# Kernel tuning notes

Measured on AMD Instinct MI355X. Metric: run time of the kernel, lower is better.

## Reference

```python
import jax, jax.numpy as jnp
import numpy as np

B, T, D = 4, 8192, 1024
N_PROTO = 8


def setup_inputs() -> dict:
    key = jax.random.key(0)
    k1, k2, k3 = jax.random.split(key, 3)
    x = jax.random.normal(k1, (B, T, D), dtype=jnp.float32)
    # torch Linear kaiming-uniform scale ~ 1/sqrt(fan_in); keeps tanh unsaturated
    W = jax.random.normal(k2, (6, D), dtype=jnp.float32) * (1.0 / np.sqrt(D))
    prototypes = jax.random.normal(k3, (N_PROTO, 6), dtype=jnp.float32)
    hamming_scale = jnp.float32(0.1)
    return {"x": x, "W": W, "prototypes": prototypes, "hamming_scale": hamming_scale}


def reference(x, W, prototypes, hamming_scale):
    # q6_project: tanh(Linear(x)) then L2-normalize with clamp(min=1e-6)
    z = jnp.tanh(jnp.einsum('btd,kd->btk', x, W))            # (B,T,6)
    z = z / jnp.clip(jnp.linalg.norm(z, axis=-1, keepdims=True), 1e-6)
    # F.normalize(prototypes, dim=-1) with eps=1e-12
    p = prototypes / jnp.clip(jnp.linalg.norm(prototypes, axis=-1, keepdims=True), 1e-12)
    dot = jnp.einsum('btk,pk->btp', z, p)                    # (B,T,P)
    dist = (6.0 - dot * 6.0) * 0.5                            # Theorem-3 Hamming distance
    return jax.nn.softmax(-hamming_scale * dist, axis=-1)    # routing weights (B,T,P)
```

## Files before the change

### kernel.cpp

```cpp
#include <hip/hip_runtime.h>


#define DIM 1024
#define NK 6
#define NPROTO 8
#define TPI 4

__global__ __launch_bounds__(256, 3) void q6_fused_kernel(
    const float* __restrict__ x,
    const float* __restrict__ W,
    const float* __restrict__ protos,
    const float* __restrict__ hs_ptr,
    float* __restrict__ out,
    int n_tokens, int n_waves)
{
    const int tid  = threadIdx.x;
    const int lane = tid & 63;
    const int wave_id = blockIdx.x * (blockDim.x >> 6) + (tid >> 6);

    __shared__ float4 wlds[NK * (DIM / 4)];
#pragma unroll
    for (int i = 0; i < (NK * DIM / 4) / 256; ++i)
        wlds[i * 256 + tid] = reinterpret_cast<const float4*>(W)[i * 256 + tid];

    const int pl = lane & 7;
    float p[NK];
#pragma unroll
    for (int k = 0; k < NK; ++k) p[k] = protos[pl * NK + k];
    {
        float pn = sqrtf(p[0]*p[0] + p[1]*p[1] + p[2]*p[2] + p[3]*p[3] + p[4]*p[4] + p[5]*p[5]);
        float inv = 1.0f / fmaxf(pn, 1e-12f);
#pragma unroll
        for (int k = 0; k < NK; ++k) p[k] *= inv;
    }
    const float hs = hs_ptr[0];

    __syncthreads();

    const bool hi5 = (lane & 32) != 0;
    const bool hi4 = (lane & 16) != 0;
    const int tloc = lane >> 4;
    const int pidx = lane & 15;

    for (int tb = wave_id * TPI; tb < n_tokens; tb += n_waves * TPI) {
        float4 xv[TPI][4];
#pragma unroll
        for (int t = 0; t < TPI; ++t) {
            const float* xt = x + (size_t)(tb + t) * DIM;
#pragma unroll
            for (int j = 0; j < 4; ++j)
                xv[t][j] = *reinterpret_cast<const float4*>(&xt[j * 256 + lane * 4]);
        }

        float acc[TPI][NK];
#pragma unroll
        for (int t = 0; t < TPI; ++t)
#pragma unroll
            for (int k = 0; k < NK; ++k) acc[t][k] = 0.0f;

#pragma unroll
        for (int j = 0; j < 4; ++j) {
            float4 wk[NK];
#pragma unroll
            for (int k = 0; k < NK; ++k)
                wk[k] = wlds[k * 256 + j * 64 + lane];
#pragma unroll
            for (int t = 0; t < TPI; ++t) {
                const float4 xvj = xv[t][j];
#pragma unroll
                for (int k = 0; k < NK; ++k) {
                    float a = acc[t][k];
                    a = fmaf(xvj.x, wk[k].x, a);
                    a = fmaf(xvj.y, wk[k].y, a);
                    a = fmaf(xvj.z, wk[k].z, a);
                    a = fmaf(xvj.w, wk[k].w, a);
                    acc[t][k] = a;
                }
            }
        }

        float r[2][NK];
#pragma unroll
        for (int tp = 0; tp < 2; ++tp)
#pragma unroll
            for (int k = 0; k < NK; ++k) {
                float send = hi5 ? acc[tp][k]     : acc[2 + tp][k];
                float keep = hi5 ? acc[2 + tp][k] : acc[tp][k];
                r[tp][k] = keep + __shfl_xor(send, 32, 64);
            }

        float z[NK];
#pragma unroll
        for (int k = 0; k < NK; ++k) {
            float send = hi4 ? r[0][k] : r[1][k];
            float keep = hi4 ? r[1][k] : r[0][k];
            z[k] = keep + __shfl_xor(send, 16, 64);
        }

#pragma unroll
        for (int off = 8; off >= 1; off >>= 1)
#pragma unroll
            for (int k = 0; k < NK; ++k)
                z[k] += __shfl_xor(z[k], off, 64);

        if (pidx < NPROTO) {
            float zz[NK];
            float nrm2 = 0.0f;
#pragma unroll
            for (int k = 0; k < NK; ++k) {
                float a = z[k];
                float e = __expf(-2.0f * fabsf(a));
                float th = (1.0f - e) / (1.0f + e);
                zz[k] = copysignf(th, a);
                nrm2 = fmaf(zz[k], zz[k], nrm2);
            }
            float inv = 1.0f / fmaxf(sqrtf(nrm2), 1e-6f);
            float dot = (zz[0]*p[0] + zz[1]*p[1] + zz[2]*p[2] +
                         zz[3]*p[3] + zz[4]*p[4] + zz[5]*p[5]) * inv;
            float logit = -hs * (6.0f - dot * 6.0f) * 0.5f;
            float m = logit;
            m = fmaxf(m, __shfl_xor(m, 1, 64));
            m = fmaxf(m, __shfl_xor(m, 2, 64));
            m = fmaxf(m, __shfl_xor(m, 4, 64));
            float e = __expf(logit - m);
            float s = e;
            s += __shfl_xor(s, 1, 64);
            s += __shfl_xor(s, 2, 64);
            s += __shfl_xor(s, 4, 64);
            out[(size_t)(tb + tloc) * NPROTO + pidx] = e / s;
        }
    }
}

extern "C" void kernel_launch(void* const* d_in, const int* in_sizes, int n_in,
                              void* d_out, int out_size, void* d_ws, size_t ws_size,
                              hipStream_t stream) {
    const float* x      = (const float*)d_in[0];
    const float* W      = (const float*)d_in[1];
    const float* protos = (const float*)d_in[2];
    const float* hs     = (const float*)d_in[3];
    float* out = (float*)d_out;

    const int n_tokens = in_sizes[0] / DIM;
    const int blocks = 1024;
    const int threads = 256;
    const int n_waves = blocks * (threads / 64);

    q6_fused_kernel<<<blocks, threads, 0, stream>>>(
        x, W, protos, hs, out, n_tokens, n_waves);
}
```

Measured before the change: 194.4 us.

## Split wave into half-wave token pairs to drop one shuffle reduction stage

Each half-wave now computes two tokens over the full hidden dimension with 8 float4 loads per token, instead of the whole wave spreading four tokens across 64 lanes. This removes the xor-32 shuffle exchange stage and halves the accumulator count per lane. Launch bounds are also raised to allow 4 blocks per CU. Per-lane x loads stay at 16 float4, but each warp-level load instruction now covers two token rows, which may change coalescing, and the tighter register budget could cause spills.

```diff
diff --git a/kernel.cpp b/kernel.cpp
--- a/kernel.cpp
+++ b/kernel.cpp
@@ -6,7 +6,7 @@
 #define NPROTO 8
 #define TPI 4
 
-__global__ __launch_bounds__(256, 3) void q6_fused_kernel(
+__global__ __launch_bounds__(256, 4) void q6_fused_kernel(
     const float* __restrict__ x,
     const float* __restrict__ W,
     const float* __restrict__ protos,
@@ -17,6 +17,8 @@
     const int tid  = threadIdx.x;
     const int lane = tid & 63;
     const int wave_id = blockIdx.x * (blockDim.x >> 6) + (tid >> 6);
+    const int h   = lane >> 5;
+    const int sub = lane & 31;
 
     __shared__ float4 wlds[NK * (DIM / 4)];
 #pragma unroll
@@ -37,35 +39,32 @@
 
     __syncthreads();
 
-    const bool hi5 = (lane & 32) != 0;
     const bool hi4 = (lane & 16) != 0;
     const int tloc = lane >> 4;
     const int pidx = lane & 15;
 
     for (int tb = wave_id * TPI; tb < n_tokens; tb += n_waves * TPI) {
-        float4 xv[TPI][4];
+        const float* xt = x + (size_t)(tb + 2 * h) * DIM + sub * 4;
+        float4 xv[2][8];
 #pragma unroll
-        for (int t = 0; t < TPI; ++t) {
-            const float* xt = x + (size_t)(tb + t) * DIM;
+        for (int j = 0; j < 8; ++j) xv[0][j] = *reinterpret_cast<const float4*>(&xt[j * 128]);
 #pragma unroll
-            for (int j = 0; j < 4; ++j)
-                xv[t][j] = *reinterpret_cast<const float4*>(&xt[j * 256 + lane * 4]);
-        }
+        for (int j = 0; j < 8; ++j) xv[1][j] = *reinterpret_cast<const float4*>(&xt[DIM + j * 128]);
 
-        float acc[TPI][NK];
+        float acc[2][NK];
 #pragma unroll
-        for (int t = 0; t < TPI; ++t)
+        for (int t = 0; t < 2; ++t)
 #pragma unroll
             for (int k = 0; k < NK; ++k) acc[t][k] = 0.0f;
 
 #pragma unroll
-        for (int j = 0; j < 4; ++j) {
+        for (int j = 0; j < 8; ++j) {
             float4 wk[NK];
 #pragma unroll
             for (int k = 0; k < NK; ++k)
-                wk[k] = wlds[k * 256 + j * 64 + lane];
+                wk[k] = wlds[k * 256 + j * 32 + sub];
 #pragma unroll
-            for (int t = 0; t < TPI; ++t) {
+            for (int t = 0; t < 2; ++t) {
                 const float4 xvj = xv[t][j];
 #pragma unroll
                 for (int k = 0; k < NK; ++k) {
@@ -79,21 +78,11 @@
             }
         }
 
-        float r[2][NK];
-#pragma unroll
-        for (int tp = 0; tp < 2; ++tp)
-#pragma unroll
-            for (int k = 0; k < NK; ++k) {
-                float send = hi5 ? acc[tp][k]     : acc[2 + tp][k];
-                float keep = hi5 ? acc[2 + tp][k] : acc[tp][k];
-                r[tp][k] = keep + __shfl_xor(send, 32, 64);
-            }
-
         float z[NK];
 #pragma unroll
         for (int k = 0; k < NK; ++k) {
-            float send = hi4 ? r[0][k] : r[1][k];
-            float keep = hi4 ? r[1][k] : r[0][k];
+            float send = hi4 ? acc[0][k] : acc[1][k];
+            float keep = hi4 ? acc[1][k] : acc[0][k];
             z[k] = keep + __shfl_xor(send, 16, 64);
         }
 
```

New measurement: 299.5 us. +54.0%, slower.
